# Kernel optimization log

Measured on AMD Instinct MI355X. Metric: run time of the kernel, lower is better.

Reference implementation:

```python
import jax, jax.numpy as jnp
import numpy as np
import math

HIDDEN = 768
NUM_HEADS = 12
HEAD_DIM = HIDDEN // NUM_HEADS
MAX_SEQ = 2048
B, S = 4, 1024


def skew_symmetric(v):
    # v: [S,3] -> [S,3,3]
    z = jnp.zeros_like(v[:, 0])
    return jnp.stack([
        jnp.stack([z, -v[:, 2], v[:, 1]], axis=-1),
        jnp.stack([v[:, 2], z, -v[:, 0]], axis=-1),
        jnp.stack([-v[:, 1], v[:, 0], z], axis=-1),
    ], axis=-2)


def se3_exp_map(xi):
    # xi: [S,6] -> R: [S,3,3], t: [S,3]  (faithful to torch so3/se3_exp_map incl. eps clamp)
    omega, v = xi[:, :3], xi[:, 3:]
    theta = jnp.clip(jnp.linalg.norm(omega, axis=1, keepdims=True), 1e-8, None)  # [S,1]
    w = omega / theta
    K = skew_symmetric(w)                       # [S,3,3]
    KK = jnp.matmul(K, K)
    I = jnp.eye(3, dtype=xi.dtype)[None]
    th = theta[:, :, None]                      # [S,1,1]
    st, ct = jnp.sin(th), jnp.cos(th)
    R = I + st * K + (1.0 - ct) * KK
    V = I + (1.0 - ct) / th**2 * K + (th - st) / th**3 * KK
    t = jnp.matmul(V, v[:, :, None])[:, :, 0]   # [S,3]
    return R, t


def setup_inputs() -> dict:
    key = jax.random.key(0)
    ks = jax.random.split(key, 6)
    x = jax.random.normal(ks[0], (B, S, HIDDEN), dtype=jnp.float32)
    # xavier_uniform bound for square [H,H]
    bound = math.sqrt(6.0 / (HIDDEN + HIDDEN))
    Wq = jax.random.uniform(ks[1], (HIDDEN, HIDDEN), minval=-bound, maxval=bound, dtype=jnp.float32)
    Wk = jax.random.uniform(ks[2], (HIDDEN, HIDDEN), minval=-bound, maxval=bound, dtype=jnp.float32)
    Wv = jax.random.uniform(ks[3], (HIDDEN, HIDDEN), minval=-bound, maxval=bound, dtype=jnp.float32)
    Wo = jax.random.uniform(ks[4], (HIDDEN, HIDDEN), minval=-bound, maxval=bound, dtype=jnp.float32)
    rotation_params = jax.random.normal(ks[5], (MAX_SEQ, 6), dtype=jnp.float32) * 0.02
    return {"x": x, "Wq": Wq, "Wk": Wk, "Wv": Wv, "Wo": Wo, "rotation_params": rotation_params}


def _forward(x, Wq, Wk, Wv, Wo, rotation_params):
    b, s, h = x.shape
    nv = h // 3  # hidden_size % 3 == 0, padding branch not taken
    R, t = se3_exp_map(rotation_params[:s])          # [s,3,3], [s,3]
    x3d = x.reshape(b, s, nv, 3)
    xr = jnp.einsum('sij,bsnj->bsni', R, x3d) + t[None, :, None, :]
    xr = xr.reshape(b, s, h)
    # Linear (no bias): y = x @ W.T
    q = jnp.einsum('bsh,oh->bso', xr, Wq).reshape(b, s, NUM_HEADS, HEAD_DIM).transpose(0, 2, 1, 3)
    k = jnp.einsum('bsh,oh->bso', xr, Wk).reshape(b, s, NUM_HEADS, HEAD_DIM).transpose(0, 2, 1, 3)
    v = jnp.einsum('bsh,oh->bso', xr, Wv).reshape(b, s, NUM_HEADS, HEAD_DIM).transpose(0, 2, 1, 3)
    scores = jnp.einsum('bhqd,bhkd->bhqk', q, k) / math.sqrt(HEAD_DIM)
    causal = jnp.tril(jnp.ones((s, s), dtype=bool))
    scores = jnp.where(causal[None, None], scores, -jnp.inf)
    attn = jax.nn.softmax(scores, axis=-1)
    out = jnp.einsum('bhqk,bhkd->bhqd', attn, v).transpose(0, 2, 1, 3).reshape(b, s, h)
    out = jnp.einsum('bsh,oh->bso', out, Wo)
    return out, attn


def reference(x, Wq, Wk, Wv, Wo, rotation_params):
    return _forward(x, Wq, Wk, Wv, Wo, rotation_params)
```

## Files before the change

### kernel.cpp

```cpp
#include <hip/hip_runtime.h>
#include <math.h>

#define S_  1024
#define H_  768
#define NH_ 12
#define HD_ 64
#define BB_ 4

typedef __bf16 bf16x8 __attribute__((ext_vector_type(8)));
typedef float f32x4 __attribute__((ext_vector_type(4)));

__device__ __forceinline__ ushort f2bf(float x) {
    unsigned u = __float_as_uint(x);
    u += 0x7FFF + ((u >> 16) & 1);
    return (ushort)(u >> 16);
}
__device__ __forceinline__ void splitbf(float x, ushort& h, ushort& l) {
    h = f2bf(x);
    float hf = __uint_as_float(((unsigned)h) << 16);
    l = f2bf(x - hf);
}
__device__ __forceinline__ f32x4 mfma16(bf16x8 a, bf16x8 b, f32x4 c) {
    return __builtin_amdgcn_mfma_f32_16x16x32_bf16(a, b, c, 0, 0, 0);
}
#define GLD16(gp, lp) __builtin_amdgcn_global_load_lds( \
    (const __attribute__((address_space(1))) unsigned int*)(gp), \
    (__attribute__((address_space(3))) unsigned int*)(lp), 16, 0, 0)

__device__ __forceinline__ bf16x8 fragld(const ushort* tile, int row, int slot) {
    return *(const bf16x8*)((const char*)tile + row * 128 + ((slot ^ (row & 7)) << 4));
}

__global__ __launch_bounds__(256)
void k_se3(const float* __restrict__ rp, float* __restrict__ Rt) {
    int s = blockIdx.x * 256 + threadIdx.x;
    if (s >= S_) return;
    float wx = rp[s * 6 + 0], wy = rp[s * 6 + 1], wz = rp[s * 6 + 2];
    float vx = rp[s * 6 + 3], vy = rp[s * 6 + 4], vz = rp[s * 6 + 5];
    float th = sqrtf(wx * wx + wy * wy + wz * wz);
    th = fmaxf(th, 1e-8f);
    float inv = 1.0f / th;
    float ux = wx * inv, uy = wy * inv, uz = wz * inv;
    float K[9] = {0.f, -uz, uy,   uz, 0.f, -ux,   -uy, ux, 0.f};
    float KK[9];
    #pragma unroll
    for (int i = 0; i < 3; ++i)
        #pragma unroll
        for (int j = 0; j < 3; ++j) {
            float acc = 0.f;
            #pragma unroll
            for (int k = 0; k < 3; ++k) acc += K[i * 3 + k] * K[k * 3 + j];
            KK[i * 3 + j] = acc;
        }
    float st = sinf(th), ct = cosf(th);
    float omc = 1.0f - ct;
    float c1 = omc / (th * th);
    float c2 = (th - st) / (th * th * th);
    float R[9], V[9];
    #pragma unroll
    for (int i = 0; i < 9; ++i) {
        float I = (i == 0 || i == 4 || i == 8) ? 1.f : 0.f;
        R[i] = I + st * K[i] + omc * KK[i];
        V[i] = I + c1 * K[i] + c2 * KK[i];
    }
    float tx = V[0] * vx + V[1] * vy + V[2] * vz;
    float ty = V[3] * vx + V[4] * vy + V[5] * vz;
    float tz = V[6] * vx + V[7] * vy + V[8] * vz;
    float* o = Rt + s * 12;
    #pragma unroll
    for (int i = 0; i < 9; ++i) o[i] = R[i];
    o[9] = tx; o[10] = ty; o[11] = tz;
}

__global__ __launch_bounds__(256)
void k_rotate_split(const float* __restrict__ x, const float* __restrict__ Rt,
                    ushort* __restrict__ xrh, ushort* __restrict__ xrl) {
    __shared__ float sR[12];
    int bs = blockIdx.x;
    int s = bs & (S_ - 1);
    if (threadIdx.x < 12) sR[threadIdx.x] = Rt[s * 12 + threadIdx.x];
    __syncthreads();
    int v = threadIdx.x;
    const float* xp = x + (size_t)bs * H_ + v * 3;
    float x0 = xp[0], x1 = xp[1], x2 = xp[2];
    float y0 = sR[0] * x0 + sR[1] * x1 + sR[2] * x2 + sR[9];
    float y1 = sR[3] * x0 + sR[4] * x1 + sR[5] * x2 + sR[10];
    float y2 = sR[6] * x0 + sR[7] * x1 + sR[8] * x2 + sR[11];
    size_t o = (size_t)bs * H_ + v * 3;
    ushort h, lo;
    splitbf(y0, h, lo); xrh[o + 0] = h; xrl[o + 0] = lo;
    splitbf(y1, h, lo); xrh[o + 1] = h; xrl[o + 1] = lo;
    splitbf(y2, h, lo); xrh[o + 2] = h; xrl[o + 2] = lo;
}

__global__ __launch_bounds__(256)
void k_wsplit(const float* __restrict__ Wq, const float* __restrict__ Wk,
              const float* __restrict__ Wv, const float* __restrict__ Wo,
              ushort* __restrict__ Wch, ushort* __restrict__ Wcl,
              ushort* __restrict__ Woh, ushort* __restrict__ Wol) {
    const int wsel = blockIdx.y;
    const float* src = (wsel == 0) ? Wq : (wsel == 1) ? Wk : (wsel == 2) ? Wv : Wo;
    const int e = (blockIdx.x * 256 + threadIdx.x) * 4;
    float4 xv = *(const float4*)(src + e);
    ushort h0, h1, h2, h3, l0, l1, l2, l3;
    splitbf(xv.x, h0, l0); splitbf(xv.y, h1, l1);
    splitbf(xv.z, h2, l2); splitbf(xv.w, h3, l3);
    ushort* dh; ushort* dl; size_t off;
    if (wsel < 3) { dh = Wch; dl = Wcl; off = (size_t)wsel * (H_ * H_) + e; }
    else          { dh = Woh; dl = Wol; off = e; }
    *(ushort4*)(dh + off) = make_ushort4(h0, h1, h2, h3);
    *(ushort4*)(dl + off) = make_ushort4(l0, l1, l2, l3);
}

template<int NF, bool QKV>
__global__ __launch_bounds__(256, 2)
void k_projsplit(const ushort* __restrict__ Ah, const ushort* __restrict__ Al,
                 const ushort* __restrict__ Bh, const ushort* __restrict__ Bl,
                 ushort* __restrict__ qh, ushort* __restrict__ ql,
                 ushort* __restrict__ kh, ushort* __restrict__ kl,
                 ushort* __restrict__ vh, ushort* __restrict__ vl,
                 float* __restrict__ outp) {
    constexpr int BN = NF * 32;
    __shared__ __align__(16) ushort sAh[128 * 64];
    __shared__ __align__(16) ushort sAl[128 * 64];
    __shared__ __align__(16) ushort sBh[BN * 64];
    __shared__ __align__(16) ushort sBl[BN * 64];
    const int mt = blockIdx.x, nt = blockIdx.y;
    const int tid = threadIdx.x, w = tid >> 6, l = tid & 63;
    const int wr = w >> 1, wc = w & 1;
    const int lrow = l >> 3;
    const int ksrc = ((l & 7) ^ lrow) * 8;
    const ushort* gsrc = (w == 0) ? Ah : (w == 1) ? Al : (w == 2) ? Bh : Bl;
    ushort* tile = (w == 0) ? sAh : (w == 1) ? sAl : (w == 2) ? sBh : sBl;
    const int nrnds = (w < 2) ? 16 : BN / 8;
    const size_t rowbase = (w < 2) ? (size_t)mt * 128 : (size_t)nt * BN;

    f32x4 acc[4][NF];
    #pragma unroll
    for (int i = 0; i < 4; ++i)
        #pragma unroll
        for (int j = 0; j < NF; ++j) acc[i][j] = (f32x4){0.f, 0.f, 0.f, 0.f};

    for (int kt = 0; kt < H_ / 64; ++kt) {
        const int k0 = kt * 64;
        #pragma unroll
        for (int r = 0; r < 16; ++r) {
            if (r < nrnds) {
                const ushort* g = gsrc + (rowbase + r * 8 + lrow) * H_ + k0 + ksrc;
                GLD16(g, (char*)tile + r * 1024);
            }
        }
        __syncthreads();
        #pragma unroll
        for (int ch = 0; ch < 2; ++ch) {
            const int slot = ch * 4 + (l >> 4);
            bf16x8 ah[4], al[4], bh[NF], bl[NF];
            #pragma unroll
            for (int mf = 0; mf < 4; ++mf) {
                int row = wr * 64 + mf * 16 + (l & 15);
                ah[mf] = fragld(sAh, row, slot);
                al[mf] = fragld(sAl, row, slot);
            }
            #pragma unroll
            for (int nf = 0; nf < NF; ++nf) {
                int row = wc * (NF * 16) + nf * 16 + (l & 15);
                bh[nf] = fragld(sBh, row, slot);
                bl[nf] = fragld(sBl, row, slot);
            }
            #pragma unroll
            for (int mf = 0; mf < 4; ++mf)
                #pragma unroll
                for (int nf = 0; nf < NF; ++nf) {
                    acc[mf][nf] = mfma16(ah[mf], bh[nf], acc[mf][nf]);
                    acc[mf][nf] = mfma16(ah[mf], bl[nf], acc[mf][nf]);
                    acc[mf][nf] = mfma16(al[mf], bh[nf], acc[mf][nf]);
                }
        }
        __syncthreads();
    }
    #pragma unroll
    for (int mf = 0; mf < 4; ++mf)
        #pragma unroll
        for (int nf = 0; nf < NF; ++nf)
            #pragma unroll
            for (int q = 0; q < 4; ++q) {
                float val = acc[mf][nf][q];
                int row = mt * 128 + wr * 64 + mf * 16 + (l >> 4) * 4 + q;
                int col = nt * BN + wc * (NF * 16) + nf * 16 + (l & 15);
                if constexpr (QKV) {
                    int which = col / H_;
                    int rem = col - which * H_;
                    int hh = rem >> 6, d = rem & 63;
                    int b = row >> 10, s = row & (S_ - 1);
                    ushort hv, lv; splitbf(val, hv, lv);
                    if (which == 2) {
                        size_t idx = ((size_t)(b * NH_ + hh) * HD_ + d) * S_ + s;
                        vh[idx] = hv; vl[idx] = lv;
                    } else {
                        size_t idx = (((size_t)(b * NH_ + hh) * S_ + s) << 6) + d;
                        ushort* dh = (which == 0) ? qh : kh;
                        ushort* dl = (which == 0) ? ql : kl;
                        dh[idx] = hv; dl[idx] = lv;
                    }
                } else {
                    outp[(size_t)row * H_ + col] = val;
                }
            }
}

__global__ __launch_bounds__(256, 2)
void k_scores(const ushort* __restrict__ qh, const ushort* __restrict__ ql,
              const ushort* __restrict__ kh, const ushort* __restrict__ kl,
              float* __restrict__ attn) {
    const int mt = blockIdx.x, nt = blockIdx.y, bh = blockIdx.z;
    if (nt > mt) return;
    __shared__ __align__(16) ushort sQh[128 * 64];
    __shared__ __align__(16) ushort sQl[128 * 64];
    __shared__ __align__(16) ushort sKh[128 * 64];
    __shared__ __align__(16) ushort sKl[128 * 64];
    const int tid = threadIdx.x, w = tid >> 6, l = tid & 63;
    const int wr = w >> 1, wc = w & 1;
    const int lrow = l >> 3, ksrc = ((l & 7) ^ lrow) * 8;
    const ushort* gsrc = (w == 0) ? qh : (w == 1) ? ql : (w == 2) ? kh : kl;
    ushort* tile = (w == 0) ? sQh : (w == 1) ? sQl : (w == 2) ? sKh : sKl;
    const size_t rowbase = (size_t)bh * S_ + (size_t)((w < 2) ? mt : nt) * 128;
    #pragma unroll
    for (int r = 0; r < 16; ++r) {
        const ushort* g = gsrc + (rowbase + r * 8 + lrow) * HD_ + ksrc;
        GLD16(g, (char*)tile + r * 1024);
    }
    f32x4 acc[4][4];
    #pragma unroll
    for (int i = 0; i < 4; ++i)
        #pragma unroll
        for (int j = 0; j < 4; ++j) acc[i][j] = (f32x4){0.f, 0.f, 0.f, 0.f};
    __syncthreads();
    #pragma unroll
    for (int ch = 0; ch < 2; ++ch) {
        const int slot = ch * 4 + (l >> 4);
        bf16x8 ah[4], al[4], bh4[4], bl4[4];
        #pragma unroll
        for (int mf = 0; mf < 4; ++mf) {
            int row = wr * 64 + mf * 16 + (l & 15);
            ah[mf] = fragld(sQh, row, slot);
            al[mf] = fragld(sQl, row, slot);
        }
        #pragma unroll
        for (int nf = 0; nf < 4; ++nf) {
            int row = wc * 64 + nf * 16 + (l & 15);
            bh4[nf] = fragld(sKh, row, slot);
            bl4[nf] = fragld(sKl, row, slot);
        }
        #pragma unroll
        for (int mf = 0; mf < 4; ++mf)
            #pragma unroll
            for (int nf = 0; nf < 4; ++nf) {
                acc[mf][nf] = mfma16(ah[mf], bh4[nf], acc[mf][nf]);
                acc[mf][nf] = mfma16(ah[mf], bl4[nf], acc[mf][nf]);
                acc[mf][nf] = mfma16(al[mf], bh4[nf], acc[mf][nf]);
            }
    }
    #pragma unroll
    for (int mf = 0; mf < 4; ++mf)
        #pragma unroll
        for (int nf = 0; nf < 4; ++nf)
            #pragma unroll
            for (int q = 0; q < 4; ++q) {
                int row = mt * 128 + wr * 64 + mf * 16 + (l >> 4) * 4 + q;
                int col = nt * 128 + wc * 64 + nf * 16 + (l & 15);
                attn[((size_t)bh << 20) + ((size_t)row << 10) + col] =
                    acc[mf][nf][q] * 0.125f;
            }
}

__global__ __launch_bounds__(256)
void k_softmax(float* __restrict__ attn) {
    const int q  = blockIdx.x;
    const int bh = blockIdx.y;
    float* row = attn + (size_t)bh * S_ * S_ + (size_t)q * S_;
    const int tid = threadIdx.x;
    __shared__ float redm[4];
    __shared__ float redl[4];
    float vals[4];
    float m = -INFINITY;
    #pragma unroll
    for (int i = 0; i < 4; ++i) {
        int j = tid + i * 256;
        vals[i] = (j <= q) ? row[j] : -INFINITY;
        m = fmaxf(m, vals[i]);
    }
    #pragma unroll
    for (int off = 32; off > 0; off >>= 1) m = fmaxf(m, __shfl_xor(m, off));
    if ((tid & 63) == 0) redm[tid >> 6] = m;
    __syncthreads();
    m = fmaxf(fmaxf(redm[0], redm[1]), fmaxf(redm[2], redm[3]));
    float lsum = 0.f;
    #pragma unroll
    for (int i = 0; i < 4; ++i) {
        int j = tid + i * 256;
        vals[i] = (j <= q) ? __expf(vals[i] - m) : 0.f;
        lsum += vals[i];
    }
    #pragma unroll
    for (int off = 32; off > 0; off >>= 1) lsum += __shfl_xor(lsum, off);
    if ((tid & 63) == 0) redl[tid >> 6] = lsum;
    __syncthreads();
    lsum = redl[0] + redl[1] + redl[2] + redl[3];
    float invl = 1.0f / lsum;
    #pragma unroll
    for (int i = 0; i < 4; ++i) {
        int j = tid + i * 256;
        row[j] = vals[i] * invl;
    }
}

__global__ __launch_bounds__(256, 2)
void k_pv(const float* __restrict__ attn, const ushort* __restrict__ vh,
          const ushort* __restrict__ vl,
          ushort* __restrict__ ctxh, ushort* __restrict__ ctxl) {
    const int mt = blockIdx.x, bh = blockIdx.y;
    __shared__ __align__(16) ushort sPh[128 * 64];
    __shared__ __align__(16) ushort sPl[128 * 64];
    __shared__ __align__(16) ushort sVh[64 * 64];
    __shared__ __align__(16) ushort sVl[64 * 64];
    const int tid = threadIdx.x, w = tid >> 6, l = tid & 63;
    const int wr = w >> 1, wc = w & 1;
    const int lrow = l >> 3, ksrc = ((l & 7) ^ lrow) * 8;
    f32x4 acc[4][2];
    #pragma unroll
    for (int i = 0; i < 4; ++i)
        #pragma unroll
        for (int j = 0; j < 2; ++j) acc[i][j] = (f32x4){0.f, 0.f, 0.f, 0.f};
    const int nsteps = (mt + 1) * 2;
    for (int kt = 0; kt < nsteps; ++kt) {
        __syncthreads();
        #pragma unroll
        for (int j = 0; j < 8; ++j) {
            int idx = j * 256 + tid;
            int row = idx >> 4, f4 = idx & 15;
            const float* src = attn + ((size_t)bh << 20)
                             + (size_t)(mt * 128 + row) * S_ + kt * 64 + f4 * 4;
            float4 xv = *(const float4*)src;
            ushort h0, h1, h2, h3, l0, l1, l2, l3;
            splitbf(xv.x, h0, l0); splitbf(xv.y, h1, l1);
            splitbf(xv.z, h2, l2); splitbf(xv.w, h3, l3);
            int addr = row * 128 + ((((f4 >> 1) ^ (row & 7))) << 4) + ((f4 & 1) << 3);
            *(ushort4*)((char*)sPh + addr) = make_ushort4(h0, h1, h2, h3);
            *(ushort4*)((char*)sPl + addr) = make_ushort4(l0, l1, l2, l3);
        }
        if (w < 2) {
            const ushort* gv = (w == 0) ? vh : vl;
            ushort* tv = (w == 0) ? sVh : sVl;
            #pragma unroll
            for (int r = 0; r < 8; ++r) {
                const ushort* g = gv + ((size_t)bh * HD_ + r * 8 + lrow) * S_
                                + kt * 64 + ksrc;
                GLD16(g, (char*)tv + r * 1024);
            }
        }
        __syncthreads();
        #pragma unroll
        for (int ch = 0; ch < 2; ++ch) {
            const int slot = ch * 4 + (l >> 4);
            bf16x8 ph[4], pl[4], bvh[2], bvl[2];
            #pragma unroll
            for (int mf = 0; mf < 4; ++mf) {
                int row = wr * 64 + mf * 16 + (l & 15);
                ph[mf] = fragld(sPh, row, slot);
                pl[mf] = fragld(sPl, row, slot);
            }
            #pragma unroll
            for (int nf = 0; nf < 2; ++nf) {
                int row = wc * 32 + nf * 16 + (l & 15);
                bvh[nf] = fragld(sVh, row, slot);
                bvl[nf] = fragld(sVl, row, slot);
            }
            #pragma unroll
            for (int mf = 0; mf < 4; ++mf)
                #pragma unroll
                for (int nf = 0; nf < 2; ++nf) {
                    acc[mf][nf] = mfma16(ph[mf], bvh[nf], acc[mf][nf]);
                    acc[mf][nf] = mfma16(ph[mf], bvl[nf], acc[mf][nf]);
                    acc[mf][nf] = mfma16(pl[mf], bvh[nf], acc[mf][nf]);
                }
        }
    }
    const int b = bh / NH_, head = bh - b * NH_;
    #pragma unroll
    for (int mf = 0; mf < 4; ++mf)
        #pragma unroll
        for (int nf = 0; nf < 2; ++nf)
            #pragma unroll
            for (int q = 0; q < 4; ++q) {
                int s = mt * 128 + wr * 64 + mf * 16 + (l >> 4) * 4 + q;
                int d = wc * 32 + nf * 16 + (l & 15);
                size_t idx = ((size_t)(b * S_ + s)) * H_ + head * HD_ + d;
                ushort hv, lv; splitbf(acc[mf][nf][q], hv, lv);
                ctxh[idx] = hv; ctxl[idx] = lv;
            }
}

extern "C" void kernel_launch(void* const* d_in, const int* in_sizes, int n_in,
                              void* d_out, int out_size, void* d_ws, size_t ws_size,
                              hipStream_t stream) {
    (void)in_sizes; (void)n_in; (void)out_size; (void)ws_size;
    const float* x  = (const float*)d_in[0];
    const float* Wq = (const float*)d_in[1];
    const float* Wk = (const float*)d_in[2];
    const float* Wv = (const float*)d_in[3];
    const float* Wo = (const float*)d_in[4];
    const float* rp = (const float*)d_in[5];

    float* out  = (float*)d_out;
    float* attn = out + (size_t)BB_ * S_ * H_;

    char* p = (char*)d_ws;
    auto alloc = [&](size_t bytes) { char* r = p; p += (bytes + 255) & ~(size_t)255; return r; };
    const size_t NE = (size_t)BB_ * S_ * H_;
    float*  Rt   = (float*) alloc(S_ * 12 * 4);
    ushort* xrh  = (ushort*)alloc(NE * 2);
    ushort* xrl  = (ushort*)alloc(NE * 2);
    ushort* Wch  = (ushort*)alloc((size_t)3 * H_ * H_ * 2);
    ushort* Wcl  = (ushort*)alloc((size_t)3 * H_ * H_ * 2);
    ushort* Woh  = (ushort*)alloc((size_t)H_ * H_ * 2);
    ushort* Wol  = (ushort*)alloc((size_t)H_ * H_ * 2);
    ushort* qh   = (ushort*)alloc(NE * 2);
    ushort* ql   = (ushort*)alloc(NE * 2);
    ushort* kh   = (ushort*)alloc(NE * 2);
    ushort* kl   = (ushort*)alloc(NE * 2);
    ushort* vh   = (ushort*)alloc(NE * 2);
    ushort* vl   = (ushort*)alloc(NE * 2);
    ushort* ctxh = xrh;
    ushort* ctxl = xrl;

    k_se3<<<dim3(4), 256, 0, stream>>>(rp, Rt);
    k_rotate_split<<<dim3(BB_ * S_), 256, 0, stream>>>(x, Rt, xrh, xrl);
    k_wsplit<<<dim3(576, 4), 256, 0, stream>>>(Wq, Wk, Wv, Wo, Wch, Wcl, Woh, Wol);

    k_projsplit<4, true><<<dim3(32, 18), 256, 0, stream>>>(
        xrh, xrl, Wch, Wcl, qh, ql, kh, kl, vh, vl, nullptr);

    k_scores<<<dim3(8, 8, BB_ * NH_), 256, 0, stream>>>(qh, ql, kh, kl, attn);
    k_softmax<<<dim3(S_, BB_ * NH_), 256, 0, stream>>>(attn);
    k_pv<<<dim3(8, BB_ * NH_), 256, 0, stream>>>(attn, vh, vl, ctxh, ctxl);

    k_projsplit<2, false><<<dim3(32, 12), 256, 0, stream>>>(
        ctxh, ctxl, Woh, Wol, nullptr, nullptr, nullptr, nullptr, nullptr, nullptr, out);
}
```

Baseline: 427.6 us.

## Drop low-order bf16 split for weights, K and V; vectorize softmax

```diff
diff --git a/kernel.cpp b/kernel.cpp
--- a/kernel.cpp
+++ b/kernel.cpp
@@ -96,44 +96,33 @@
 __global__ __launch_bounds__(256)
 void k_wsplit(const float* __restrict__ Wq, const float* __restrict__ Wk,
               const float* __restrict__ Wv, const float* __restrict__ Wo,
-              ushort* __restrict__ Wch, ushort* __restrict__ Wcl,
-              ushort* __restrict__ Woh, ushort* __restrict__ Wol) {
+              ushort* __restrict__ Wch, ushort* __restrict__ Woh) {
     const int wsel = blockIdx.y;
     const float* src = (wsel == 0) ? Wq : (wsel == 1) ? Wk : (wsel == 2) ? Wv : Wo;
     const int e = (blockIdx.x * 256 + threadIdx.x) * 4;
     float4 xv = *(const float4*)(src + e);
-    ushort h0, h1, h2, h3, l0, l1, l2, l3;
-    splitbf(xv.x, h0, l0); splitbf(xv.y, h1, l1);
-    splitbf(xv.z, h2, l2); splitbf(xv.w, h3, l3);
-    ushort* dh; ushort* dl; size_t off;
-    if (wsel < 3) { dh = Wch; dl = Wcl; off = (size_t)wsel * (H_ * H_) + e; }
-    else          { dh = Woh; dl = Wol; off = e; }
-    *(ushort4*)(dh + off) = make_ushort4(h0, h1, h2, h3);
-    *(ushort4*)(dl + off) = make_ushort4(l0, l1, l2, l3);
+    ushort4 hv = make_ushort4(f2bf(xv.x), f2bf(xv.y), f2bf(xv.z), f2bf(xv.w));
+    if (wsel < 3) *(ushort4*)(Wch + (size_t)wsel * (H_ * H_) + e) = hv;
+    else          *(ushort4*)(Woh + e) = hv;
 }
 
 template<int NF, bool QKV>
 __global__ __launch_bounds__(256, 2)
-void k_projsplit(const ushort* __restrict__ Ah, const ushort* __restrict__ Al,
-                 const ushort* __restrict__ Bh, const ushort* __restrict__ Bl,
-                 ushort* __restrict__ qh, ushort* __restrict__ ql,
-                 ushort* __restrict__ kh, ushort* __restrict__ kl,
-                 ushort* __restrict__ vh, ushort* __restrict__ vl,
-                 float* __restrict__ outp) {
+void k_proj2(const ushort* __restrict__ Ah, const ushort* __restrict__ Al,
+             const ushort* __restrict__ Bh,
+             ushort* __restrict__ qh, ushort* __restrict__ ql,
+             ushort* __restrict__ kh, ushort* __restrict__ vh,
+             float* __restrict__ outp) {
     constexpr int BN = NF * 32;
+    constexpr int TOT = 32 + BN / 8;
     __shared__ __align__(16) ushort sAh[128 * 64];
     __shared__ __align__(16) ushort sAl[128 * 64];
     __shared__ __align__(16) ushort sBh[BN * 64];
-    __shared__ __align__(16) ushort sBl[BN * 64];
     const int mt = blockIdx.x, nt = blockIdx.y;
     const int tid = threadIdx.x, w = tid >> 6, l = tid & 63;
     const int wr = w >> 1, wc = w & 1;
     const int lrow = l >> 3;
     const int ksrc = ((l & 7) ^ lrow) * 8;
-    const ushort* gsrc = (w == 0) ? Ah : (w == 1) ? Al : (w == 2) ? Bh : Bl;
-    ushort* tile = (w == 0) ? sAh : (w == 1) ? sAl : (w == 2) ? sBh : sBl;
-    const int nrnds = (w < 2) ? 16 : BN / 8;
-    const size_t rowbase = (w < 2) ? (size_t)mt * 128 : (size_t)nt * BN;
 
     f32x4 acc[4][NF];
     #pragma unroll
@@ -143,18 +132,20 @@
 
     for (int kt = 0; kt < H_ / 64; ++kt) {
         const int k0 = kt * 64;
-        #pragma unroll
-        for (int r = 0; r < 16; ++r) {
-            if (r < nrnds) {
-                const ushort* g = gsrc + (rowbase + r * 8 + lrow) * H_ + k0 + ksrc;
-                GLD16(g, (char*)tile + r * 1024);
-            }
+        for (int rr = w; rr < TOT; rr += 4) {
+            int t = (rr < 16) ? 0 : (rr < 32) ? 1 : 2;
+            int r = rr - ((rr < 16) ? 0 : (rr < 32) ? 16 : 32);
+            const ushort* src = (t == 0) ? Ah : (t == 1) ? Al : Bh;
+            size_t rowb = (t < 2) ? (size_t)mt * 128 : (size_t)nt * BN;
+            const ushort* g = src + (rowb + r * 8 + lrow) * H_ + k0 + ksrc;
+            ushort* dstt = (t == 0) ? sAh : (t == 1) ? sAl : sBh;
+            GLD16(g, dstt + r * 512);
         }
         __syncthreads();
         #pragma unroll
         for (int ch = 0; ch < 2; ++ch) {
             const int slot = ch * 4 + (l >> 4);
-            bf16x8 ah[4], al[4], bh[NF], bl[NF];
+            bf16x8 ah[4], al[4], bh[NF];
             #pragma unroll
             for (int mf = 0; mf < 4; ++mf) {
                 int row = wr * 64 + mf * 16 + (l & 15);
@@ -162,17 +153,13 @@
                 al[mf] = fragld(sAl, row, slot);
             }
             #pragma unroll
-            for (int nf = 0; nf < NF; ++nf) {
-                int row = wc * (NF * 16) + nf * 16 + (l & 15);
-                bh[nf] = fragld(sBh, row, slot);
-                bl[nf] = fragld(sBl, row, slot);
-            }
+            for (int nf = 0; nf < NF; ++nf)
+                bh[nf] = fragld(sBh, wc * (NF * 16) + nf * 16 + (l & 15), slot);
             #pragma unroll
             for (int mf = 0; mf < 4; ++mf)
                 #pragma unroll
                 for (int nf = 0; nf < NF; ++nf) {
                     acc[mf][nf] = mfma16(ah[mf], bh[nf], acc[mf][nf]);
-                    acc[mf][nf] = mfma16(ah[mf], bl[nf], acc[mf][nf]);
                     acc[mf][nf] = mfma16(al[mf], bh[nf], acc[mf][nf]);
                 }
         }
@@ -192,15 +179,14 @@
                     int rem = col - which * H_;
                     int hh = rem >> 6, d = rem & 63;
                     int b = row >> 10, s = row & (S_ - 1);
-                    ushort hv, lv; splitbf(val, hv, lv);
                     if (which == 2) {
-                        size_t idx = ((size_t)(b * NH_ + hh) * HD_ + d) * S_ + s;
-                        vh[idx] = hv; vl[idx] = lv;
+                        vh[((size_t)(b * NH_ + hh) * HD_ + d) * S_ + s] = f2bf(val);
+                    } else if (which == 1) {
+                        kh[(((size_t)(b * NH_ + hh) * S_ + s) << 6) + d] = f2bf(val);
                     } else {
                         size_t idx = (((size_t)(b * NH_ + hh) * S_ + s) << 6) + d;
-                        ushort* dh = (which == 0) ? qh : kh;
-                        ushort* dl = (which == 0) ? ql : kl;
-                        dh[idx] = hv; dl[idx] = lv;
+                        ushort hv, lv; splitbf(val, hv, lv);
+                        qh[idx] = hv; ql[idx] = lv;
                     }
                 } else {
                     outp[(size_t)row * H_ + col] = val;
@@ -210,24 +196,23 @@
 
 __global__ __launch_bounds__(256, 2)
 void k_scores(const ushort* __restrict__ qh, const ushort* __restrict__ ql,
-              const ushort* __restrict__ kh, const ushort* __restrict__ kl,
-              float* __restrict__ attn) {
+              const ushort* __restrict__ kh, float* __restrict__ attn) {
     const int mt = blockIdx.x, nt = blockIdx.y, bh = blockIdx.z;
     if (nt > mt) return;
     __shared__ __align__(16) ushort sQh[128 * 64];
     __shared__ __align__(16) ushort sQl[128 * 64];
     __shared__ __align__(16) ushort sKh[128 * 64];
-    __shared__ __align__(16) ushort sKl[128 * 64];
     const int tid = threadIdx.x, w = tid >> 6, l = tid & 63;
     const int wr = w >> 1, wc = w & 1;
     const int lrow = l >> 3, ksrc = ((l & 7) ^ lrow) * 8;
-    const ushort* gsrc = (w == 0) ? qh : (w == 1) ? ql : (w == 2) ? kh : kl;
-    ushort* tile = (w == 0) ? sQh : (w == 1) ? sQl : (w == 2) ? sKh : sKl;
-    const size_t rowbase = (size_t)bh * S_ + (size_t)((w < 2) ? mt : nt) * 128;
-    #pragma unroll
-    for (int r = 0; r < 16; ++r) {
-        const ushort* g = gsrc + (rowbase + r * 8 + lrow) * HD_ + ksrc;
-        GLD16(g, (char*)tile + r * 1024);
+    for (int rr = w; rr < 48; rr += 4) {
+        int t = (rr < 16) ? 0 : (rr < 32) ? 1 : 2;
+        int r = rr - ((rr < 16) ? 0 : (rr < 32) ? 16 : 32);
+        const ushort* src = (t == 0) ? qh : (t == 1) ? ql : kh;
+        size_t rowb = (size_t)bh * S_ + (size_t)((t < 2) ? mt : nt) * 128;
+        const ushort* g = src + (rowb + r * 8 + lrow) * HD_ + ksrc;
+        ushort* dstt = (t == 0) ? sQh : (t == 1) ? sQl : sKh;
+        GLD16(g, dstt + r * 512);
     }
     f32x4 acc[4][4];
     #pragma unroll
@@ -238,7 +223,7 @@
     #pragma unroll
     for (int ch = 0; ch < 2; ++ch) {
         const int slot = ch * 4 + (l >> 4);
-        bf16x8 ah[4], al[4], bh4[4], bl4[4];
+        bf16x8 ah[4], al[4], bh4[4];
         #pragma unroll
         for (int mf = 0; mf < 4; ++mf) {
             int row = wr * 64 + mf * 16 + (l & 15);
@@ -246,17 +231,13 @@
             al[mf] = fragld(sQl, row, slot);
         }
         #pragma unroll
-        for (int nf = 0; nf < 4; ++nf) {
-            int row = wc * 64 + nf * 16 + (l & 15);
-            bh4[nf] = fragld(sKh, row, slot);
-            bl4[nf] = fragld(sKl, row, slot);
-        }
+        for (int nf = 0; nf < 4; ++nf)
+            bh4[nf] = fragld(sKh, wc * 64 + nf * 16 + (l & 15), slot);
         #pragma unroll
         for (int mf = 0; mf < 4; ++mf)
             #pragma unroll
             for (int nf = 0; nf < 4; ++nf) {
                 acc[mf][nf] = mfma16(ah[mf], bh4[nf], acc[mf][nf]);
-                acc[mf][nf] = mfma16(ah[mf], bl4[nf], acc[mf][nf]);
                 acc[mf][nf] = mfma16(al[mf], bh4[nf], acc[mf][nf]);
             }
     }
@@ -277,52 +258,41 @@
 void k_softmax(float* __restrict__ attn) {
     const int q  = blockIdx.x;
     const int bh = blockIdx.y;
-    float* row = attn + (size_t)bh * S_ * S_ + (size_t)q * S_;
+    float* row = attn + ((size_t)bh << 20) + ((size_t)q << 10);
     const int tid = threadIdx.x;
+    const int j0 = tid * 4;
     __shared__ float redm[4];
     __shared__ float redl[4];
-    float vals[4];
-    float m = -INFINITY;
-    #pragma unroll
-    for (int i = 0; i < 4; ++i) {
-        int j = tid + i * 256;
-        vals[i] = (j <= q) ? row[j] : -INFINITY;
-        m = fmaxf(m, vals[i]);
-    }
+    float4 v = *(const float4*)(row + j0);
+    float x0 = (j0 + 0 <= q) ? v.x : -INFINITY;
+    float x1 = (j0 + 1 <= q) ? v.y : -INFINITY;
+    float x2 = (j0 + 2 <= q) ? v.z : -INFINITY;
+    float x3 = (j0 + 3 <= q) ? v.w : -INFINITY;
+    float m = fmaxf(fmaxf(x0, x1), fmaxf(x2, x3));
     #pragma unroll
     for (int off = 32; off > 0; off >>= 1) m = fmaxf(m, __shfl_xor(m, off));
     if ((tid & 63) == 0) redm[tid >> 6] = m;
     __syncthreads();
     m = fmaxf(fmaxf(redm[0], redm[1]), fmaxf(redm[2], redm[3]));
-    float lsum = 0.f;
-    #pragma unroll
-    for (int i = 0; i < 4; ++i) {
-        int j = tid + i * 256;
-        vals[i] = (j <= q) ? __expf(vals[i] - m) : 0.f;
-        lsum += vals[i];
-    }
+    float e0 = __expf(x0 - m), e1 = __expf(x1 - m);
+    float e2 = __expf(x2 - m), e3 = __expf(x3 - m);
+    float lsum = (e0 + e1) + (e2 + e3);
     #pragma unroll
     for (int off = 32; off > 0; off >>= 1) lsum += __shfl_xor(lsum, off);
     if ((tid & 63) == 0) redl[tid >> 6] = lsum;
     __syncthreads();
     lsum = redl[0] + redl[1] + redl[2] + redl[3];
     float invl = 1.0f / lsum;
-    #pragma unroll
-    for (int i = 0; i < 4; ++i) {
-        int j = tid + i * 256;
-        row[j] = vals[i] * invl;
-    }
+    *(float4*)(row + j0) = make_float4(e0 * invl, e1 * invl, e2 * invl, e3 * invl);
 }
 
 __global__ __launch_bounds__(256, 2)
 void k_pv(const float* __restrict__ attn, const ushort* __restrict__ vh,
-          const ushort* __restrict__ vl,
           ushort* __restrict__ ctxh, ushort* __restrict__ ctxl) {
     const int mt = blockIdx.x, bh = blockIdx.y;
     __shared__ __align__(16) ushort sPh[128 * 64];
     __shared__ __align__(16) ushort sPl[128 * 64];
     __shared__ __align__(16) ushort sVh[64 * 64];
-    __shared__ __align__(16) ushort sVl[64 * 64];
     const int tid = threadIdx.x, w = tid >> 6, l = tid & 63;
     const int wr = w >> 1, wc = w & 1;
     const int lrow = l >> 3, ksrc = ((l & 7) ^ lrow) * 8;
@@ -348,21 +318,16 @@
             *(ushort4*)((char*)sPh + addr) = make_ushort4(h0, h1, h2, h3);
             *(ushort4*)((char*)sPl + addr) = make_ushort4(l0, l1, l2, l3);
         }
-        if (w < 2) {
-            const ushort* gv = (w == 0) ? vh : vl;
-            ushort* tv = (w == 0) ? sVh : sVl;
-            #pragma unroll
-            for (int r = 0; r < 8; ++r) {
-                const ushort* g = gv + ((size_t)bh * HD_ + r * 8 + lrow) * S_
-                                + kt * 64 + ksrc;
-                GLD16(g, (char*)tv + r * 1024);
-            }
+        for (int rr = w; rr < 8; rr += 4) {
+            const ushort* g = vh + ((size_t)bh * HD_ + rr * 8 + lrow) * S_
+                            + kt * 64 + ksrc;
+            GLD16(g, sVh + rr * 512);
         }
         __syncthreads();
         #pragma unroll
         for (int ch = 0; ch < 2; ++ch) {
             const int slot = ch * 4 + (l >> 4);
-            bf16x8 ph[4], pl[4], bvh[2], bvl[2];
+            bf16x8 ph[4], pl[4], bvh[2];
             #pragma unroll
             for (int mf = 0; mf < 4; ++mf) {
                 int row = wr * 64 + mf * 16 + (l & 15);
@@ -370,17 +335,13 @@
                 pl[mf] = fragld(sPl, row, slot);
             }
             #pragma unroll
-            for (int nf = 0; nf < 2; ++nf) {
-                int row = wc * 32 + nf * 16 + (l & 15);
-                bvh[nf] = fragld(sVh, row, slot);
-                bvl[nf] = fragld(sVl, row, slot);
-            }
+            for (int nf = 0; nf < 2; ++nf)
+                bvh[nf] = fragld(sVh, wc * 32 + nf * 16 + (l & 15), slot);
             #pragma unroll
             for (int mf = 0; mf < 4; ++mf)
                 #pragma unroll
                 for (int nf = 0; nf < 2; ++nf) {
                     acc[mf][nf] = mfma16(ph[mf], bvh[nf], acc[mf][nf]);
-                    acc[mf][nf] = mfma16(ph[mf], bvl[nf], acc[mf][nf]);
                     acc[mf][nf] = mfma16(pl[mf], bvh[nf], acc[mf][nf]);
                 }
         }
@@ -421,29 +382,25 @@
     ushort* xrh  = (ushort*)alloc(NE * 2);
     ushort* xrl  = (ushort*)alloc(NE * 2);
     ushort* Wch  = (ushort*)alloc((size_t)3 * H_ * H_ * 2);
-    ushort* Wcl  = (ushort*)alloc((size_t)3 * H_ * H_ * 2);
     ushort* Woh  = (ushort*)alloc((size_t)H_ * H_ * 2);
-    ushort* Wol  = (ushort*)alloc((size_t)H_ * H_ * 2);
     ushort* qh   = (ushort*)alloc(NE * 2);
     ushort* ql   = (ushort*)alloc(NE * 2);
     ushort* kh   = (ushort*)alloc(NE * 2);
-    ushort* kl   = (ushort*)alloc(NE * 2);
     ushort* vh   = (ushort*)alloc(NE * 2);
-    ushort* vl   = (ushort*)alloc(NE * 2);
     ushort* ctxh = xrh;
     ushort* ctxl = xrl;
 
     k_se3<<<dim3(4), 256, 0, stream>>>(rp, Rt);
     k_rotate_split<<<dim3(BB_ * S_), 256, 0, stream>>>(x, Rt, xrh, xrl);
-    k_wsplit<<<dim3(576, 4), 256, 0, stream>>>(Wq, Wk, Wv, Wo, Wch, Wcl, Woh, Wol);
-
-    k_projsplit<4, true><<<dim3(32, 18), 256, 0, stream>>>(
-        xrh, xrl, Wch, Wcl, qh, ql, kh, kl, vh, vl, nullptr);
-
-    k_scores<<<dim3(8, 8, BB_ * NH_), 256, 0, stream>>>(qh, ql, kh, kl, attn);
+    k_wsplit<<<dim3(576, 4), 256, 0, stream>>>(Wq, Wk, Wv, Wo, Wch, Woh);
+
+    k_proj2<4, true><<<dim3(32, 18), 256, 0, stream>>>(
+        xrh, xrl, Wch, qh, ql, kh, vh, nullptr);
+
+    k_scores<<<dim3(8, 8, BB_ * NH_), 256, 0, stream>>>(qh, ql, kh, attn);
     k_softmax<<<dim3(S_, BB_ * NH_), 256, 0, stream>>>(attn);
-    k_pv<<<dim3(8, BB_ * NH_), 256, 0, stream>>>(attn, vh, vl, ctxh, ctxl);
-
-    k_projsplit<2, false><<<dim3(32, 12), 256, 0, stream>>>(
-        ctxh, ctxl, Woh, Wol, nullptr, nullptr, nullptr, nullptr, nullptr, nullptr, out);
-}
+    k_pv<<<dim3(8, BB_ * NH_), 256, 0, stream>>>(attn, vh, ctxh, ctxl);
+
+    k_proj2<2, false><<<dim3(32, 12), 256, 0, stream>>>(
+        ctxh, ctxl, Woh, nullptr, nullptr, nullptr, nullptr, out);
+}
```

Measured after the change: 412.2 us. 3.6% less time.
